# Optimization experiments

Measured on AMD Instinct MI355X. Metric: run time of the kernel, lower is better.

## Reference

```python
import jax, jax.numpy as jnp
import numpy as np

DILATION = (1, 1)


def pd_indexing2d(x, dh, dw, dilation):
    """Pitch-dependent indexing. x:(B,C,H,W); dh,dw:(B,1,W) -> list of 9 (B,C,H,W)."""
    B, C, H, W = x.shape
    # dilation factors, clamped to >= 1, broadcast to (B,1,1,W)
    dil_h = jnp.maximum((dh * dilation[0]).astype(jnp.int32), 1)[:, :, None, :]
    dil_w = jnp.maximum((dw * dilation[1]).astype(jnp.int32), 1)[:, :, None, :]

    rH = jnp.arange(H)[None, None, :, None]   # (1,1,H,1)
    cW = jnp.arange(W)[None, None, None, :]   # (1,1,1,W)

    # row (frequency) indices
    idxD = jnp.abs(rH - dil_h) % H            # (B,1,H,W)
    up = rH + dil_h
    idxU = jnp.where(up >= H, rH, up)         # overflow -> idxU - dil = base
    rows = [idxD, jnp.broadcast_to(rH, (1, 1, H, 1)), idxU]

    # col (time) indices
    idxL = jnp.abs(cW - dil_w) % W            # (B,1,1,W)
    rt = cW + dil_w
    # torch uses negative index -(rt % W) - 1 == W - 1 - (rt % W)
    idxR = jnp.where(rt >= W, W - 1 - (rt % W), rt)
    cols = [idxL, jnp.broadcast_to(cW, (1, 1, 1, W)), idxR]

    bidx = jnp.arange(B).reshape(B, 1, 1, 1)
    cidx = jnp.arange(C).reshape(1, C, 1, 1)
    xs = []
    for r in rows:
        for c in cols:
            xs.append(x[bidx, cidx, r, c])
    return xs


def setup_inputs() -> dict:
    key = jax.random.key(0)
    k1, k2, k3, k4, k5 = jax.random.split(key, 5)
    B, C, O, H, W = 8, 64, 64, 80, 800
    x = jax.random.normal(k1, (B, C, H, W), dtype=jnp.float32)
    dh = jax.random.randint(k2, (B, 1, W), 1, 4).astype(jnp.float32)
    dw = jax.random.randint(k3, (B, 1, W), 1, 4).astype(jnp.float32)
    weight = jax.random.normal(k4, (9, O, C), dtype=jnp.float32) * 0.05
    bias = jax.random.normal(k5, (O,), dtype=jnp.float32) * 0.05
    return {"x": x, "dh": dh, "dw": dw, "weight": weight, "bias": bias}


def reference(x, dh, dw, weight, bias):
    xs = pd_indexing2d(x, dh, dw, DILATION)
    out = jnp.einsum('bchw,oc->bohw', xs[0], weight[0]) + bias[None, :, None, None]
    for k in range(1, 9):
        out = out + jnp.einsum('bchw,oc->bohw', xs[k], weight[k])
    return out
```

## Files before the change

### kernel.cpp

```cpp
#include <hip/hip_runtime.h>

#define B_  8
#define C_  64
#define O_  64
#define H_  80
#define W_  800
#define NCHM   25

#define ROWS_  10
#define ROWPX_ 44
#define ROWB_  (ROWPX_ * 128)
#define LDSX_BYTES (ROWS_ * ROWB_)
#define NTASK  3520

typedef short bf16x8 __attribute__((ext_vector_type(8)));
typedef float f32x4  __attribute__((ext_vector_type(4)));

__device__ __forceinline__ unsigned short f2bf(float f) {
    unsigned int u = __float_as_uint(f);
    unsigned int r = u + 0x7FFFu + ((u >> 16) & 1u);
    return (unsigned short)(r >> 16);
}

__global__ void k_wfrag(const float* __restrict__ wt, unsigned short* __restrict__ wf) {
    const int t = blockIdx.x * 256 + threadIdx.x;
    const int j    = t & 7;
    const int lane = (t >> 3) & 63;
    const int mt   = (t >> 9) & 3;
    const int ks   = t >> 11;
    const int tap  = ks >> 1, hf = ks & 1;
    const int o = mt * 16 + (lane & 15);
    const int c = hf * 32 + (lane >> 4) * 8 + j;
    wf[t] = f2bf(wt[(tap * 64 + o) * 64 + c]);
}

__global__ void __launch_bounds__(512, 4)
k_main(const float* __restrict__ x,
       const unsigned short* __restrict__ wfrag,
       const float* __restrict__ dh, const float* __restrict__ dw,
       const float* __restrict__ bias, float* __restrict__ out) {
    __shared__ char lx[LDSX_BYTES];
    const int tid  = threadIdx.x;
    const int wave = tid >> 6, lane = tid & 63;

    const unsigned int flat = blockIdx.x;
    const int b = flat & 7;
    const unsigned int l = flat >> 3;
    const int chunk = l % NCHM;
    const int hq    = l / NCHM;
    const int h0 = hq * 4;
    const int w0 = chunk * 32;
    const int h   = h0 + (wave & 3);
    const int mtb = (wave >> 2) * 2;
    const int l15 = lane & 15, kq = lane >> 4;

    {
        const int wq0 = w0 - 4;
#pragma unroll
        for (int it = 0; it < 7; ++it) {
            const int T = tid + it * 512;
            if (T < NTASK) {
                const int row = T / 352;
                const int rem = T - row * 352;
                const int cp  = rem / 11;
                const int q   = rem - cp * 11;
                const int p0  = 4 * q;
                const int ca  = wq0 + p0;
                if (ca >= 0 && ca + 3 < W_) {
                    int ar = h0 - 3 + row;
                    ar = ar < 0 ? 0 : (ar > H_ - 1 ? H_ - 1 : ar);
                    const int c0 = 2 * cp;
                    const float* s0 = x + ((size_t)(b * C_ + c0) * H_ + ar) * W_ + ca;
                    const f32x4 v0 = *(const f32x4*)s0;
                    const f32x4 v1 = *(const f32x4*)(s0 + (size_t)(H_ * W_));
                    const int g = cp >> 2, widx = cp & 3;
                    char* rbase = lx + row * ROWB_ + widx * 4;
#pragma unroll
                    for (int i = 0; i < 4; ++i) {
                        const unsigned int u = (unsigned int)f2bf(v0[i])
                                             | ((unsigned int)f2bf(v1[i]) << 16);
                        *(unsigned int*)(rbase + (p0 + i) * 128
                                         + (((g + ca + i) & 7) << 4)) = u;
                    }
                }
            }
        }
    }

    unsigned int rowb[2][3], colb[2][3];
#pragma unroll
    for (int nt = 0; nt < 2; ++nt) {
        const int pw  = w0 + nt * 16 + l15;
        const int dhi = (int)dh[b * W_ + pw];
        const int dwi = (int)dw[b * W_ + pw];
        int rD = h - dhi;   if (rD < 0) rD = -rD;
        const int rU = (h + dhi < H_) ? (h + dhi) : h;
        int cL = pw - dwi;  if (cL < 0) cL = -cL;
        const int cR = (pw + dwi < W_) ? (pw + dwi) : (2 * W_ - 1 - pw - dwi);
        rowb[nt][0] = (unsigned int)(rD - h0 + 3) * ROWB_;
        rowb[nt][1] = (unsigned int)(h  - h0 + 3) * ROWB_;
        rowb[nt][2] = (unsigned int)(rU - h0 + 3) * ROWB_;
        const int cs[3] = {cL, pw, cR};
#pragma unroll
        for (int j = 0; j < 3; ++j)
            colb[nt][j] = (unsigned int)(cs[j] - (w0 - 4)) * 128u
                        + (unsigned int)(((cs[j] + kq) & 7) * 16);
    }

    const char* wfb = (const char*)wfrag;
    const unsigned int aoff = (unsigned int)lane * 16u;

    f32x4 acc[2][2];
#pragma unroll
    for (int mtl = 0; mtl < 2; ++mtl) {
        const f32x4 bv = *(const f32x4*)(bias + (mtb + mtl) * 16 + kq * 4);
#pragma unroll
        for (int nt = 0; nt < 2; ++nt)
#pragma unroll
            for (int r = 0; r < 4; ++r) acc[mtl][nt][r] = bv[r];
    }

    __syncthreads();

    bf16x8 bcur[2], bnxt[2], a0[2], a1[2], a2[2];
#pragma unroll
    for (int nt = 0; nt < 2; ++nt)
        bcur[nt] = *(const bf16x8*)(lx + rowb[nt][0] + colb[nt][0]);
#pragma unroll
    for (int mtl = 0; mtl < 2; ++mtl) {
        a0[mtl] = *(const bf16x8*)(wfb + (unsigned int)((0 * 4 + mtb + mtl) * 1024) + aoff);
        a1[mtl] = *(const bf16x8*)(wfb + (unsigned int)((1 * 4 + mtb + mtl) * 1024) + aoff);
    }

#pragma unroll
    for (int s = 0; s < 18; ++s) {
        if (s < 17) {
            const int sn = s + 1;
            const int tap = sn >> 1, hf = sn & 1;
            const int i = tap / 3, j = tap % 3;
#pragma unroll
            for (int nt = 0; nt < 2; ++nt) {
                unsigned int a = rowb[nt][i] + colb[nt][j];
                if (hf) a ^= 64u;
                bnxt[nt] = *(const bf16x8*)(lx + a);
            }
        }
        if (s < 16) {
#pragma unroll
            for (int mtl = 0; mtl < 2; ++mtl)
                a2[mtl] = *(const bf16x8*)(wfb
                            + (unsigned int)(((s + 2) * 4 + mtb + mtl) * 1024) + aoff);
        }
#pragma unroll
        for (int mtl = 0; mtl < 2; ++mtl)
#pragma unroll
            for (int nt = 0; nt < 2; ++nt)
                acc[mtl][nt] = __builtin_amdgcn_mfma_f32_16x16x32_bf16(
                    a0[mtl], bcur[nt], acc[mtl][nt], 0, 0, 0);
#pragma unroll
        for (int nt = 0; nt < 2; ++nt) bcur[nt] = bnxt[nt];
#pragma unroll
        for (int mtl = 0; mtl < 2; ++mtl) { a0[mtl] = a1[mtl]; a1[mtl] = a2[mtl]; }
    }

#pragma unroll
    for (int mtl = 0; mtl < 2; ++mtl) {
#pragma unroll
        for (int nt = 0; nt < 2; ++nt) {
            const int w = w0 + nt * 16 + l15;
            const unsigned int ob =
                ((unsigned int)(b * O_ + (mtb + mtl) * 16 + kq * 4) * (unsigned int)H_
                 + (unsigned int)h) * (unsigned int)W_ + (unsigned int)w;
#pragma unroll
            for (int r = 0; r < 4; ++r)
                out[ob + (unsigned int)r * 64000u] = acc[mtl][nt][r];
        }
    }
}

extern "C" void kernel_launch(void* const* d_in, const int* in_sizes, int n_in,
                              void* d_out, int out_size, void* d_ws, size_t ws_size,
                              hipStream_t stream) {
    const float* x      = (const float*)d_in[0];
    const float* dh     = (const float*)d_in[1];
    const float* dw     = (const float*)d_in[2];
    const float* weight = (const float*)d_in[3];
    const float* bias   = (const float*)d_in[4];
    float* out = (float*)d_out;

    unsigned short* wfrag = (unsigned short*)d_ws;

    k_wfrag<<<dim3(144), 256, 0, stream>>>(weight, wfrag);
    k_main<<<dim3(NCHM * (H_ / 4) * B_), 512, 0, stream>>>(x, wfrag, dh, dw, bias, out);
}
```

Measured before the change: 292.2 us.

## Restructure LDS staging: 8-channel tasks, batched loads, 16-byte stores, padded rows

```diff
diff --git a/kernel.cpp b/kernel.cpp
--- a/kernel.cpp
+++ b/kernel.cpp
@@ -9,9 +9,9 @@
 
 #define ROWS_  10
 #define ROWPX_ 44
-#define ROWB_  (ROWPX_ * 128)
-#define LDSX_BYTES (ROWS_ * ROWB_)
-#define NTASK  3520
+#define ROWB_  5648u
+#define LDSX_BYTES (ROWS_ * 5648)
+#define NTASK  880
 
 typedef short bf16x8 __attribute__((ext_vector_type(8)));
 typedef float f32x4  __attribute__((ext_vector_type(4)));
@@ -39,7 +39,7 @@
        const unsigned short* __restrict__ wfrag,
        const float* __restrict__ dh, const float* __restrict__ dw,
        const float* __restrict__ bias, float* __restrict__ out) {
-    __shared__ char lx[LDSX_BYTES];
+    __shared__ __attribute__((aligned(16))) char lx[LDSX_BYTES];
     const int tid  = threadIdx.x;
     const int wave = tid >> 6, lane = tid & 63;
 
@@ -55,33 +55,45 @@
     const int l15 = lane & 15, kq = lane >> 4;
 
     {
-        const int wq0 = w0 - 4;
-#pragma unroll
-        for (int it = 0; it < 7; ++it) {
+        f32x4 v[2][8];
+        int ok[2];
+        unsigned int wb[2];
+        int swz[2];
+#pragma unroll
+        for (int it = 0; it < 2; ++it) {
             const int T = tid + it * 512;
+            ok[it] = 0;
             if (T < NTASK) {
-                const int row = T / 352;
-                const int rem = T - row * 352;
-                const int cp  = rem / 11;
-                const int q   = rem - cp * 11;
-                const int p0  = 4 * q;
-                const int ca  = wq0 + p0;
+                const int row = T % 10;
+                const int q   = (T / 10) % 11;
+                const int g   = T / 110;
+                const int ca  = w0 - 4 + 4 * q;
                 if (ca >= 0 && ca + 3 < W_) {
+                    ok[it] = 1;
                     int ar = h0 - 3 + row;
                     ar = ar < 0 ? 0 : (ar > H_ - 1 ? H_ - 1 : ar);
-                    const int c0 = 2 * cp;
-                    const float* s0 = x + ((size_t)(b * C_ + c0) * H_ + ar) * W_ + ca;
-                    const f32x4 v0 = *(const f32x4*)s0;
-                    const f32x4 v1 = *(const f32x4*)(s0 + (size_t)(H_ * W_));
-                    const int g = cp >> 2, widx = cp & 3;
-                    char* rbase = lx + row * ROWB_ + widx * 4;
-#pragma unroll
-                    for (int i = 0; i < 4; ++i) {
-                        const unsigned int u = (unsigned int)f2bf(v0[i])
-                                             | ((unsigned int)f2bf(v1[i]) << 16);
-                        *(unsigned int*)(rbase + (p0 + i) * 128
-                                         + (((g + ca + i) & 7) << 4)) = u;
-                    }
+                    const float* s0 = x + ((size_t)(b * C_ + g * 8) * H_ + ar) * W_ + ca;
+#pragma unroll
+                    for (int c = 0; c < 8; ++c)
+                        v[it][c] = *(const f32x4*)(s0 + (size_t)c * (H_ * W_));
+                    wb[it]  = (unsigned int)row * ROWB_ + (unsigned int)(4 * q) * 128u;
+                    swz[it] = g + ca;
+                }
+            }
+        }
+#pragma unroll
+        for (int it = 0; it < 2; ++it) {
+            if (ok[it]) {
+#pragma unroll
+                for (int i = 0; i < 4; ++i) {
+                    unsigned int u[4];
+#pragma unroll
+                    for (int j = 0; j < 4; ++j)
+                        u[j] = (unsigned int)f2bf(v[it][2 * j][i])
+                             | ((unsigned int)f2bf(v[it][2 * j + 1][i]) << 16);
+                    char* dst = lx + wb[it] + (unsigned int)(i * 128)
+                              + (unsigned int)(((swz[it] + i) & 7) << 4);
+                    *(uint4*)dst = make_uint4(u[0], u[1], u[2], u[3]);
                 }
             }
         }
@@ -140,9 +152,8 @@
             const int i = tap / 3, j = tap % 3;
 #pragma unroll
             for (int nt = 0; nt < 2; ++nt) {
-                unsigned int a = rowb[nt][i] + colb[nt][j];
-                if (hf) a ^= 64u;
-                bnxt[nt] = *(const bf16x8*)(lx + a);
+                const unsigned int cb = colb[nt][j] ^ (hf ? 64u : 0u);
+                bnxt[nt] = *(const bf16x8*)(lx + rowb[nt][i] + cb);
             }
         }
         if (s < 16) {
```

After: 328.8 us. +12.5%, slower.
